# Kernel optimization log

Measured on AMD Instinct MI355X. Metric: run time of the kernel, lower is better.

## Reference

```python
import jax, jax.numpy as jnp
from jax import lax
import numpy as np

NUM_HEADS = 8
KW = 3  # window kernel size

def _avgpool3(x):
    # x: [B,C,H,W]; AvgPool2d(3,1,1) with count_include_pad=True -> sum/9
    s = lax.reduce_window(x, 0.0, lax.add, (1, 1, KW, KW), (1, 1, 1, 1),
                          ((0, 0), (0, 0), (1, 1), (1, 1)))
    return s / (KW * KW)

def _unfold3(y):
    # y: [B,h,w,C] -> [B,h,w,9,C]; patch index ordered row-major (kh,kw)
    B, h, w, C = y.shape
    yp = jnp.pad(y, ((0, 0), (1, 1), (1, 1), (0, 0)))
    return jnp.stack([yp[:, i:i + h, j:j + w, :]
                      for i in range(KW) for j in range(KW)], axis=3)

def setup_inputs():
    key = jax.random.key(0)
    ks = jax.random.split(key, 9)
    B, C, H, W = 8, 256, 64, 64
    sd = 0.02
    return {
        "x": jax.random.normal(ks[0], (B, C, H, W), jnp.float32),
        "W_qkv": jax.random.normal(ks[1], (4 * C, C), jnp.float32) * sd,
        "b_qkv": jnp.zeros((4 * C,), jnp.float32),
        "W1": jax.random.normal(ks[2], (C // 2, C), jnp.float32) * sd,
        "b1": jnp.zeros((C // 2,), jnp.float32),
        "W2": jax.random.normal(ks[3], (C, C // 2), jnp.float32) * sd,
        "b2": jnp.zeros((C,), jnp.float32),
        "Wp": jax.random.normal(ks[4], (C, C), jnp.float32) * sd,
        "bp": jnp.zeros((C,), jnp.float32),
    }

def reference(x, W_qkv, b_qkv, W1, b1, W2, b2, Wp, bp):
    B, C, H, W = x.shape
    nH = NUM_HEADS
    hd = C // nH
    scale = hd ** -0.5
    # avg pool (stride 1 keeps spatial dims), to channels-last
    y = _avgpool3(x).transpose(0, 2, 3, 1)                 # [B,h,w,C]
    qkv = y @ W_qkv.T + b_qkv                              # [B,h,w,4C]
    qkv = qkv.reshape(B, H, W, C, 4)
    q, k, v, chans = qkv[..., 0], qkv[..., 1], qkv[..., 2], qkv[..., 3]
    # channel gate
    g = jax.nn.sigmoid(jax.nn.relu(chans @ W1.T + b1) @ W2.T + b2)  # [B,h,w,C]
    # local window attention: each query attends to its 3x3 neighborhood
    qh = q.reshape(B, H, W, nH, hd)                        # [B,h,w,n,d]
    kp = _unfold3(k).reshape(B, H, W, KW * KW, nH, hd)     # [B,h,w,9,n,d]
    vp = _unfold3(v).reshape(B, H, W, KW * KW, nH, hd)
    attn = jnp.einsum('bhwnd,bhwknd->bhwnk', qh, kp) * scale
    attn = jax.nn.softmax(attn, axis=-1)
    out = jnp.einsum('bhwnk,bhwknd->bhwnd', attn, vp).reshape(B, H, W, C)
    out = out * g + out
    out = out @ Wp.T + bp
    return out.transpose(0, 3, 1, 2)                       # [B,C,H,W]
```

## Files before the change

### kernel.cpp

```cpp
#include <hip/hip_runtime.h>
#include <stdint.h>

typedef __bf16    bf16x8 __attribute__((ext_vector_type(8)));
typedef float     f32x4  __attribute__((ext_vector_type(4)));
typedef uint32_t  u32x4  __attribute__((ext_vector_type(4)));

#define MFMA(a,b,c) __builtin_amdgcn_mfma_f32_16x16x32_bf16((a),(b),(c),0,0,0)

__device__ __align__(16) uint16_t g_y [8*64*64*256];
__device__ __align__(16) uint16_t g_ao[8*64*64*256];
__device__ __align__(16) uint16_t g_ch[8*64*64*256];
__device__ __align__(16) uint16_t g_wpk[393216];

#define WQF 0
#define WKF 65536
#define WVF 131072
#define WCF 196608
#define W1F 262144
#define W2F 294912
#define WPF 327680

static __device__ __forceinline__ float b2f(uint32_t u){ return __builtin_bit_cast(float, u<<16); }
static __device__ __forceinline__ uint32_t f2b(float f){
  uint32_t x = __builtin_bit_cast(uint32_t, f);
  return (x + 0x7fffu + ((x>>16)&1u)) >> 16;
}

__global__ __launch_bounds__(256) void kpack(const float* __restrict__ Wqkv,
    const float* __restrict__ W1, const float* __restrict__ W2,
    const float* __restrict__ Wp){
  int idx = blockIdx.x*256 + threadIdx.x;
  int j = idx & 7, lane = (idx>>3)&63;
  int n16 = lane & 15, q4 = lane>>4;
  float v;
  if (idx < 262144){
    int t = idx >> 16, l = idx & 65535;
    int s = (l>>9)&7, nt = l>>12;
    v = Wqkv[(4*(nt*16+n16) + t)*256 + s*32 + q4*8 + j];
  } else if (idx < 294912){
    int l = idx - 262144;
    int s = (l>>9)&7, nt = l>>12;
    v = W1[(nt*16+n16)*256 + s*32 + q4*8 + j];
  } else if (idx < 327680){
    int l = idx - 294912;
    int s = (l>>9)&3, nt = l>>11;
    v = W2[(nt*16+n16)*128 + s*32 + q4*8 + j];
  } else {
    int l = idx - 327680;
    int s = (l>>9)&7, nt = l>>12;
    v = Wp[(nt*16+n16)*256 + s*32 + q4*8 + j];
  }
  g_wpk[idx] = (uint16_t)f2b(v);
}

__global__ __launch_bounds__(512) void kpool(const float* __restrict__ x){
  __shared__ __align__(16) uint16_t sm[3*256*82];
  uint32_t* smw = (uint32_t*)sm;
  int t = threadIdx.x;
  int b = blockIdx.x >> 6, h = blockIdx.x & 63;
  for (int i=t; i<3*256*41; i+=512) smw[i] = 0;
  __syncthreads();
  #pragma unroll
  for (int i=0;i<24;i++){
    int id = t + 512*i;
    int w4 = id&15, c = (id>>4)&255, hh = id>>12;
    int gy = h - 1 + hh;
    if ((unsigned)gy < 64u){
      f32x4 ld = *(const f32x4*)&x[(((b*256+c)*64+gy)*64) + w4*4];
      int wb = (((hh*256+c)*82 + 8 + w4*4) >> 1);
      smw[wb+0] = f2b(ld[0]) | (f2b(ld[1])<<16);
      smw[wb+1] = f2b(ld[2]) | (f2b(ld[3])<<16);
    }
  }
  __syncthreads();
  int c = t & 255, wsel = t >> 8;
  int r0 = c*82, r1 = r0 + 256*82, r2 = r1 + 256*82;
  int w0 = wsel*32;
  float csp = b2f(sm[r0+w0+7]) + b2f(sm[r1+w0+7]) + b2f(sm[r2+w0+7]);
  float csc = b2f(sm[r0+w0+8]) + b2f(sm[r1+w0+8]) + b2f(sm[r2+w0+8]);
  uint16_t* dst = g_y + ((b*64+h)*64)*256 + c;
  for (int j2=0;j2<32;j2++){
    int w = w0 + j2;
    float csn = b2f(sm[r0+w+9]) + b2f(sm[r1+w+9]) + b2f(sm[r2+w+9]);
    float yv = (csp + csc + csn) * (1.0f/9.0f);
    dst[w*256] = (uint16_t)f2b(yv);
    csp = csc; csc = csn;
  }
}

#define YSTR 264
#define HSTR 134
#define K2_QS 26400
#define K2_KS 34976
#define K2_VS 48376
__global__ __launch_bounds__(512,2) void kattn(const float* __restrict__ bqkv){
  __shared__ __align__(16) uint16_t sm[61776];
  int t = threadIdx.x;
  int lane = t & 63, wave = t >> 6;
  int n16 = lane & 15, quad = lane >> 4;
  int bb = blockIdx.x >> 6, ty = (blockIdx.x>>3)&7, tx = blockIdx.x & 7;

  {
    uint32_t* smw = (uint32_t*)sm;
    for (int i=t; i<30888; i+=512) smw[i] = 0;
  }
  __syncthreads();

  #pragma unroll
  for (int i=0;i<7;i++){
    int id = t + 512*i;
    if (id < 3200){
      int hp = id >> 5, c8 = id & 31;
      int py = hp/10, px = hp - py*10;
      int gy = ty*8 + py - 1, gx = tx*8 + px - 1;
      u32x4 ld = {0,0,0,0};
      if ((unsigned)gy<64u && (unsigned)gx<64u)
        ld = *(const u32x4*)&g_y[((bb*64+gy)*64+gx)*256 + c8*8];
      *(u32x4*)&sm[hp*YSTR + c8*8] = ld;
    }
  }
  __syncthreads();

  for (int hf=0; hf<2; hf++){
    {
      int ntg = hf*8 + wave;
      bf16x8 Bq[8];
      #pragma unroll
      for (int s=0;s<8;s++) Bq[s] = *(const bf16x8*)&g_wpk[WQF + ((ntg*8+s)*64+lane)*8];
      float bq = bqkv[4*(ntg*16+n16) + 0];
      int colB = wave*16;
      #pragma unroll
      for (int mt=0; mt<4; mt++){
        f32x4 a = {0.f,0.f,0.f,0.f};
        int m = mt*16 + n16;
        int hrow = 10*(m>>3) + (m&7) + 11;
        #pragma unroll
        for (int s=0;s<8;s++){
          bf16x8 A = *(const bf16x8*)&sm[hrow*YSTR + s*32 + quad*8];
          a = MFMA(A, Bq[s], a);
        }
        #pragma unroll
        for (int r=0;r<4;r++){
          int row = mt*16 + quad*4 + r;
          sm[K2_QS + row*HSTR + colB + n16] = (uint16_t)f2b(a[r] + bq);
        }
      }
    }
    __syncthreads();
    {
      int ntg = hf*8 + wave;
      bf16x8 Bk[8], Bv[8];
      #pragma unroll
      for (int s=0;s<8;s++){
        Bk[s] = *(const bf16x8*)&g_wpk[WKF + ((ntg*8+s)*64+lane)*8];
        Bv[s] = *(const bf16x8*)&g_wpk[WVF + ((ntg*8+s)*64+lane)*8];
      }
      float bk = bqkv[4*(ntg*16+n16) + 1];
      float bv = bqkv[4*(ntg*16+n16) + 2];
      int colB = wave*16;
      #pragma unroll
      for (int mt=0; mt<7; mt++){
        f32x4 ak = {0.f,0.f,0.f,0.f}, av = {0.f,0.f,0.f,0.f};
        int m = mt*16 + n16;
        int mr = (m < 100) ? m : 99;
        #pragma unroll
        for (int s=0;s<8;s++){
          bf16x8 A = *(const bf16x8*)&sm[mr*YSTR + s*32 + quad*8];
          ak = MFMA(A, Bk[s], ak);
          av = MFMA(A, Bv[s], av);
        }
        #pragma unroll
        for (int r=0;r<4;r++){
          int row = mt*16 + quad*4 + r;
          if (row < 100){
            int py = row/10, px = row - py*10;
            int gy = ty*8 + py - 1, gx = tx*8 + px - 1;
            bool ok = ((unsigned)gy<64u) && ((unsigned)gx<64u);
            float vk = ok ? ak[r] + bk : 0.f;
            float vv = ok ? av[r] + bv : 0.f;
            sm[K2_KS + row*HSTR + colB + n16] = (uint16_t)f2b(vk);
            sm[K2_VS + row*HSTR + colB + n16] = (uint16_t)f2b(vv);
          }
        }
      }
    }
    __syncthreads();
    if (t < 256){
      int p = t & 63, hl = t >> 6;
      int iy = p >> 3, ix = p & 7;
      int cb = hl*32;
      const uint32_t* q32 = (const uint32_t*)&sm[K2_QS + p*HSTR + cb];
      float qv[32];
      #pragma unroll
      for (int i=0;i<16;i++){ uint32_t u=q32[i]; qv[2*i]=b2f(u&0xffffu); qv[2*i+1]=b2f(u>>16); }
      int hb = (iy+1)*10 + ix + 1;
      const int off[9] = {-11,-10,-9,-1,0,1,9,10,11};
      float sc[9];
      #pragma unroll
      for (int nb=0;nb<9;nb++){
        const uint32_t* k32 = (const uint32_t*)&sm[K2_KS + (hb+off[nb])*HSTR + cb];
        float s = 0.f;
        #pragma unroll
        for (int i=0;i<16;i++){ uint32_t u=k32[i]; s += qv[2*i]*b2f(u&0xffffu) + qv[2*i+1]*b2f(u>>16); }
        sc[nb] = s * 0.17677669529663687f;
      }
      float mx = sc[0];
      #pragma unroll
      for (int nb=1;nb<9;nb++) mx = fmaxf(mx, sc[nb]);
      float l = 0.f;
      #pragma unroll
      for (int nb=0;nb<9;nb++){ sc[nb] = __expf(sc[nb]-mx); l += sc[nb]; }
      float inv = 1.f / l;
      float o[32];
      #pragma unroll
      for (int i=0;i<32;i++) o[i]=0.f;
      #pragma unroll
      for (int nb=0;nb<9;nb++){
        float wgt = sc[nb]*inv;
        const uint32_t* v32 = (const uint32_t*)&sm[K2_VS + (hb+off[nb])*HSTR + cb];
        #pragma unroll
        for (int i=0;i<16;i++){ uint32_t u=v32[i]; o[2*i] += wgt*b2f(u&0xffffu); o[2*i+1] += wgt*b2f(u>>16); }
      }
      int pg = ((bb*64 + ty*8+iy)*64 + tx*8+ix);
      uint16_t* dst = g_ao + pg*256 + hf*128 + cb;
      #pragma unroll
      for (int i=0;i<4;i++){
        u32x4 stv;
        #pragma unroll
        for (int jj=0;jj<4;jj++) stv[jj] = f2b(o[i*8+2*jj]) | (f2b(o[i*8+2*jj+1])<<16);
        *(u32x4*)&dst[i*8] = stv;
      }
    }
    __syncthreads();
  }
  #pragma unroll
  for (int jj=0;jj<2;jj++){
    int ntg = wave*2 + jj;
    bf16x8 Bc[8];
    #pragma unroll
    for (int s=0;s<8;s++) Bc[s] = *(const bf16x8*)&g_wpk[WCF + ((ntg*8+s)*64+lane)*8];
    float bc = bqkv[4*(ntg*16+n16) + 3];
    int colB = ntg*16;
    #pragma unroll
    for (int mt=0; mt<4; mt++){
      f32x4 a = {0.f,0.f,0.f,0.f};
      int m = mt*16 + n16;
      int hrow = 10*(m>>3) + (m&7) + 11;
      #pragma unroll
      for (int s=0;s<8;s++){
        bf16x8 A = *(const bf16x8*)&sm[hrow*YSTR + s*32 + quad*8];
        a = MFMA(A, Bc[s], a);
      }
      #pragma unroll
      for (int r=0;r<4;r++){
        int row = mt*16 + quad*4 + r;
        sm[K2_QS + row*264 + colB + n16] = (uint16_t)f2b(a[r] + bc);
      }
    }
  }
  __syncthreads();
  #pragma unroll
  for (int i=0;i<4;i++){
    int id = t + 512*i;
    int row = id >> 5, c8 = id & 31;
    u32x4 ld = *(const u32x4*)&sm[K2_QS + row*264 + c8*8];
    int iy = row>>3, ix = row&7;
    int pg = ((bb*64 + ty*8+iy)*64 + tx*8+ix);
    *(u32x4*)&g_ch[pg*256 + c8*8] = ld;
  }
}

#define K3_CH 0
#define K3_HS 16896
#define K3_AO 25600
__global__ __launch_bounds__(512,2) void kout(const float* __restrict__ b1,
    const float* __restrict__ b2v, const float* __restrict__ bp,
    float* __restrict__ out){
  __shared__ __align__(16) uint16_t sm[42496];
  int t = threadIdx.x;
  int lane = t & 63, wave = t >> 6;
  int n16 = lane & 15, quad = lane >> 4;
  int b = blockIdx.x >> 6, h = blockIdx.x & 63;
  int pix0 = blockIdx.x * 64;
  {
    uint32_t* smw = (uint32_t*)sm;
    for (int i=t; i<21248; i+=512) smw[i] = 0;
  }
  __syncthreads();
  #pragma unroll
  for (int i=0;i<4;i++){
    int id = t + 512*i;
    int row = id >> 5, c8 = id & 31;
    *(u32x4*)&sm[K3_CH + row*264 + c8*8] = *(const u32x4*)&g_ch[(pix0+row)*256 + c8*8];
    *(u32x4*)&sm[K3_AO + row*264 + c8*8] = *(const u32x4*)&g_ao[(pix0+row)*256 + c8*8];
  }
  __syncthreads();
  {
    int ntg = wave;
    bf16x8 Bf[8];
    #pragma unroll
    for (int s=0;s<8;s++) Bf[s] = *(const bf16x8*)&g_wpk[W1F + ((ntg*8+s)*64+lane)*8];
    float bs = b1[ntg*16+n16];
    int colB = wave*16;
    #pragma unroll
    for (int mt=0;mt<4;mt++){
      f32x4 a = {0.f,0.f,0.f,0.f};
      #pragma unroll
      for (int s=0;s<8;s++){
        bf16x8 A = *(const bf16x8*)&sm[K3_CH + (mt*16+n16)*264 + s*32 + quad*8];
        a = MFMA(A, Bf[s], a);
      }
      #pragma unroll
      for (int r=0;r<4;r++){
        int row = mt*16 + quad*4 + r;
        sm[K3_HS + row*136 + colB + n16] = (uint16_t)f2b(fmaxf(a[r]+bs, 0.f));
      }
    }
  }
  __syncthreads();
  #pragma unroll
  for (int jj=0;jj<2;jj++){
    int ntg = wave*2 + jj;
    bf16x8 Bf[4];
    #pragma unroll
    for (int s=0;s<4;s++) Bf[s] = *(const bf16x8*)&g_wpk[W2F + ((ntg*4+s)*64+lane)*8];
    float bs = b2v[ntg*16+n16];
    int colB = ntg*16;
    #pragma unroll
    for (int mt=0;mt<4;mt++){
      f32x4 a = {0.f,0.f,0.f,0.f};
      #pragma unroll
      for (int s=0;s<4;s++){
        bf16x8 A = *(const bf16x8*)&sm[K3_HS + (mt*16+n16)*136 + s*32 + quad*8];
        a = MFMA(A, Bf[s], a);
      }
      #pragma unroll
      for (int r=0;r<4;r++){
        int row = mt*16 + quad*4 + r;
        float gg = 1.f/(1.f+__expf(-(a[r] + bs)));
        float ao = b2f((uint32_t)sm[K3_AO + row*264 + colB + n16]);
        sm[K3_CH + row*264 + colB + n16] = (uint16_t)f2b(ao*(1.f+gg));
      }
    }
  }
  __syncthreads();
  #pragma unroll
  for (int jj=0;jj<2;jj++){
    int ntg = wave*2 + jj;
    bf16x8 Bf[8];
    #pragma unroll
    for (int s=0;s<8;s++) Bf[s] = *(const bf16x8*)&g_wpk[WPF + ((ntg*8+s)*64+lane)*8];
    float bs = bp[ntg*16+n16];
    int colB = ntg*16;
    #pragma unroll
    for (int mt=0;mt<4;mt++){
      f32x4 a = {0.f,0.f,0.f,0.f};
      #pragma unroll
      for (int s=0;s<8;s++){
        bf16x8 A = *(const bf16x8*)&sm[K3_CH + (mt*16+n16)*264 + s*32 + quad*8];
        a = MFMA(A, Bf[s], a);
      }
      #pragma unroll
      for (int r=0;r<4;r++){
        int row = mt*16 + quad*4 + r;
        sm[K3_AO + row*264 + colB + n16] = (uint16_t)f2b(a[r]+bs);
      }
    }
  }
  __syncthreads();
  #pragma unroll
  for (int i=0;i<8;i++){
    int idx = t + 512*i;
    int c = idx >> 4, wc = idx & 15;
    f32x4 stv;
    #pragma unroll
    for (int j=0;j<4;j++) stv[j] = b2f((uint32_t)sm[K3_AO + (wc*4+j)*264 + c]);
    *(f32x4*)&out[(((b*256)+c)*64 + h)*64 + wc*4] = stv;
  }
}

extern "C" void kernel_launch(void* const* d_in, const int* in_sizes, int n_in,
                              void* d_out, int out_size, void* d_ws, size_t ws_size,
                              hipStream_t stream){
  (void)in_sizes; (void)n_in; (void)d_ws; (void)ws_size; (void)out_size;
  const float* x    = (const float*)d_in[0];
  const float* Wqkv = (const float*)d_in[1];
  const float* bqkv = (const float*)d_in[2];
  const float* W1   = (const float*)d_in[3];
  const float* b1   = (const float*)d_in[4];
  const float* W2   = (const float*)d_in[5];
  const float* b2   = (const float*)d_in[6];
  const float* Wp   = (const float*)d_in[7];
  const float* bp   = (const float*)d_in[8];
  kpack<<<dim3(1536), dim3(256), 0, stream>>>(Wqkv, W1, W2, Wp);
  kpool<<<dim3(512),  dim3(512), 0, stream>>>(x);
  kattn<<<dim3(512),  dim3(512), 0, stream>>>(bqkv);
  kout <<<dim3(512),  dim3(512), 0, stream>>>(b1, b2, bp, (float*)d_out);
}
```

Before: 217.8 us.

## Fuse output MLP/gate/projection into attention kernel, drop global intermediates

Merges the kout kernel into kattn, so the attention output and channel-branch activations stay in registers and shared memory instead of round-tripping through the g_ao/g_ch global buffers. The channel projection now runs on waves 4-7 while waves 0-3 compute attention, overlapping the two. The change also trims the full shared-memory zeroing in kpool and kattn to only the padding that is needed, and remaps block indices for tile locality. The cost is higher register pressure from the held opk/chp arrays, and the output store is now 8x8-tile shaped, which is less contiguous.

Measured after the change: 188.4 us. 1.16x faster.

```diff
diff --git a/kernel.cpp b/kernel.cpp
--- a/kernel.cpp
+++ b/kernel.cpp
@@ -8,8 +8,6 @@
 #define MFMA(a,b,c) __builtin_amdgcn_mfma_f32_16x16x32_bf16((a),(b),(c),0,0,0)
 
 __device__ __align__(16) uint16_t g_y [8*64*64*256];
-__device__ __align__(16) uint16_t g_ao[8*64*64*256];
-__device__ __align__(16) uint16_t g_ch[8*64*64*256];
 __device__ __align__(16) uint16_t g_wpk[393216];
 
 #define WQF 0
@@ -58,8 +56,15 @@
   uint32_t* smw = (uint32_t*)sm;
   int t = threadIdx.x;
   int b = blockIdx.x >> 6, h = blockIdx.x & 63;
-  for (int i=t; i<3*256*41; i+=512) smw[i] = 0;
-  __syncthreads();
+  for (int i=t; i<768; i+=512){
+    int base = i*41;
+    smw[base+3]  = 0;
+    smw[base+36] = 0;
+  }
+  if (h==0 || h==63){
+    int hh = (h==0) ? 0 : 2;
+    for (int i=t; i<10496; i+=512) smw[hh*10496 + i] = 0;
+  }
   #pragma unroll
   for (int i=0;i<24;i++){
     int id = t + 512*i;
@@ -93,18 +98,22 @@
 #define K2_QS 26400
 #define K2_KS 34976
 #define K2_VS 48376
-__global__ __launch_bounds__(512,2) void kattn(const float* __restrict__ bqkv){
+#define MCH 0
+#define MHS 16896
+#define MAO 25600
+__global__ __launch_bounds__(512,2) void kattn(const float* __restrict__ bqkv,
+    const float* __restrict__ b1, const float* __restrict__ b2v,
+    const float* __restrict__ bp, float* __restrict__ out){
   __shared__ __align__(16) uint16_t sm[61776];
   int t = threadIdx.x;
   int lane = t & 63, wave = t >> 6;
   int n16 = lane & 15, quad = lane >> 4;
-  int bb = blockIdx.x >> 6, ty = (blockIdx.x>>3)&7, tx = blockIdx.x & 7;
-
-  {
-    uint32_t* smw = (uint32_t*)sm;
-    for (int i=t; i<30888; i+=512) smw[i] = 0;
-  }
-  __syncthreads();
+  int bid = blockIdx.x;
+  int bb = bid>>6, tyhi=(bid>>4)&3, txl=(bid>>3)&1, tylo=(bid>>2)&1, txp=bid&3;
+  int ty = tyhi*2+tylo, tx = txp*2+txl;
+
+  uint32_t opk[2][16];
+  uint32_t chp[32];
 
   #pragma unroll
   for (int i=0;i<7;i++){
@@ -121,6 +130,7 @@
   }
   __syncthreads();
 
+  #pragma unroll
   for (int hf=0; hf<2; hf++){
     {
       int ntg = hf*8 + wave;
@@ -185,8 +195,8 @@
       }
     }
     __syncthreads();
-    if (t < 256){
-      int p = t & 63, hl = t >> 6;
+    if (wave < 4){
+      int p = t & 63, hl = wave;
       int iy = p >> 3, ix = p & 7;
       int cb = hl*32;
       const uint32_t* q32 = (const uint32_t*)&sm[K2_QS + p*HSTR + cb];
@@ -221,80 +231,57 @@
         #pragma unroll
         for (int i=0;i<16;i++){ uint32_t u=v32[i]; o[2*i] += wgt*b2f(u&0xffffu); o[2*i+1] += wgt*b2f(u>>16); }
       }
-      int pg = ((bb*64 + ty*8+iy)*64 + tx*8+ix);
-      uint16_t* dst = g_ao + pg*256 + hf*128 + cb;
-      #pragma unroll
-      for (int i=0;i<4;i++){
-        u32x4 stv;
-        #pragma unroll
-        for (int jj=0;jj<4;jj++) stv[jj] = f2b(o[i*8+2*jj]) | (f2b(o[i*8+2*jj+1])<<16);
-        *(u32x4*)&dst[i*8] = stv;
+      #pragma unroll
+      for (int i=0;i<16;i++) opk[hf][i] = f2b(o[2*i]) | (f2b(o[2*i+1])<<16);
+    } else if (hf == 0){
+      #pragma unroll
+      for (int jj=0;jj<4;jj++){
+        int ntg = (wave-4)*4 + jj;
+        bf16x8 Bc[8];
+        #pragma unroll
+        for (int s=0;s<8;s++) Bc[s] = *(const bf16x8*)&g_wpk[WCF + ((ntg*8+s)*64+lane)*8];
+        float bc = bqkv[4*(ntg*16+n16) + 3];
+        #pragma unroll
+        for (int mt=0; mt<4; mt++){
+          f32x4 a = {0.f,0.f,0.f,0.f};
+          int m = mt*16 + n16;
+          int hrow = 10*(m>>3) + (m&7) + 11;
+          #pragma unroll
+          for (int s=0;s<8;s++){
+            bf16x8 A = *(const bf16x8*)&sm[hrow*YSTR + s*32 + quad*8];
+            a = MFMA(A, Bc[s], a);
+          }
+          chp[(jj*4+mt)*2+0] = f2b(a[0]+bc) | (f2b(a[1]+bc)<<16);
+          chp[(jj*4+mt)*2+1] = f2b(a[2]+bc) | (f2b(a[3]+bc)<<16);
+        }
+      }
+    } else {
+      #pragma unroll
+      for (int jj=0;jj<4;jj++){
+        int ntg = (wave-4)*4 + jj;
+        int col = ntg*16 + n16;
+        #pragma unroll
+        for (int mt=0;mt<4;mt++){
+          #pragma unroll
+          for (int r2=0;r2<2;r2++){
+            uint32_t v = chp[(jj*4+mt)*2+r2];
+            int row = mt*16 + quad*4 + r2*2;
+            sm[MCH + row*264 + col]     = (uint16_t)(v & 0xffffu);
+            sm[MCH + (row+1)*264 + col] = (uint16_t)(v >> 16);
+          }
+        }
       }
     }
     __syncthreads();
   }
-  #pragma unroll
-  for (int jj=0;jj<2;jj++){
-    int ntg = wave*2 + jj;
-    bf16x8 Bc[8];
-    #pragma unroll
-    for (int s=0;s<8;s++) Bc[s] = *(const bf16x8*)&g_wpk[WCF + ((ntg*8+s)*64+lane)*8];
-    float bc = bqkv[4*(ntg*16+n16) + 3];
-    int colB = ntg*16;
-    #pragma unroll
-    for (int mt=0; mt<4; mt++){
-      f32x4 a = {0.f,0.f,0.f,0.f};
-      int m = mt*16 + n16;
-      int hrow = 10*(m>>3) + (m&7) + 11;
-      #pragma unroll
-      for (int s=0;s<8;s++){
-        bf16x8 A = *(const bf16x8*)&sm[hrow*YSTR + s*32 + quad*8];
-        a = MFMA(A, Bc[s], a);
-      }
-      #pragma unroll
-      for (int r=0;r<4;r++){
-        int row = mt*16 + quad*4 + r;
-        sm[K2_QS + row*264 + colB + n16] = (uint16_t)f2b(a[r] + bc);
-      }
-    }
-  }
-  __syncthreads();
-  #pragma unroll
-  for (int i=0;i<4;i++){
-    int id = t + 512*i;
-    int row = id >> 5, c8 = id & 31;
-    u32x4 ld = *(const u32x4*)&sm[K2_QS + row*264 + c8*8];
-    int iy = row>>3, ix = row&7;
-    int pg = ((bb*64 + ty*8+iy)*64 + tx*8+ix);
-    *(u32x4*)&g_ch[pg*256 + c8*8] = ld;
-  }
-}
-
-#define K3_CH 0
-#define K3_HS 16896
-#define K3_AO 25600
-__global__ __launch_bounds__(512,2) void kout(const float* __restrict__ b1,
-    const float* __restrict__ b2v, const float* __restrict__ bp,
-    float* __restrict__ out){
-  __shared__ __align__(16) uint16_t sm[42496];
-  int t = threadIdx.x;
-  int lane = t & 63, wave = t >> 6;
-  int n16 = lane & 15, quad = lane >> 4;
-  int b = blockIdx.x >> 6, h = blockIdx.x & 63;
-  int pix0 = blockIdx.x * 64;
-  {
-    uint32_t* smw = (uint32_t*)sm;
-    for (int i=t; i<21248; i+=512) smw[i] = 0;
-  }
-  __syncthreads();
-  #pragma unroll
-  for (int i=0;i<4;i++){
-    int id = t + 512*i;
-    int row = id >> 5, c8 = id & 31;
-    *(u32x4*)&sm[K3_CH + row*264 + c8*8] = *(const u32x4*)&g_ch[(pix0+row)*256 + c8*8];
-    *(u32x4*)&sm[K3_AO + row*264 + c8*8] = *(const u32x4*)&g_ao[(pix0+row)*256 + c8*8];
-  }
-  __syncthreads();
+  if (wave < 4){
+    int p = t & 63, cb = wave*32;
+    #pragma unroll
+    for (int hf=0;hf<2;hf++)
+      #pragma unroll
+      for (int i=0;i<16;i++)
+        *(uint32_t*)&sm[MAO + p*264 + hf*128 + cb + 2*i] = opk[hf][i];
+  }
   {
     int ntg = wave;
     bf16x8 Bf[8];
@@ -307,13 +294,13 @@
       f32x4 a = {0.f,0.f,0.f,0.f};
       #pragma unroll
       for (int s=0;s<8;s++){
-        bf16x8 A = *(const bf16x8*)&sm[K3_CH + (mt*16+n16)*264 + s*32 + quad*8];
+        bf16x8 A = *(const bf16x8*)&sm[MCH + (mt*16+n16)*264 + s*32 + quad*8];
         a = MFMA(A, Bf[s], a);
       }
       #pragma unroll
       for (int r=0;r<4;r++){
         int row = mt*16 + quad*4 + r;
-        sm[K3_HS + row*136 + colB + n16] = (uint16_t)f2b(fmaxf(a[r]+bs, 0.f));
+        sm[MHS + row*136 + colB + n16] = (uint16_t)f2b(fmaxf(a[r]+bs, 0.f));
       }
     }
   }
@@ -331,15 +318,15 @@
       f32x4 a = {0.f,0.f,0.f,0.f};
       #pragma unroll
       for (int s=0;s<4;s++){
-        bf16x8 A = *(const bf16x8*)&sm[K3_HS + (mt*16+n16)*136 + s*32 + quad*8];
+        bf16x8 A = *(const bf16x8*)&sm[MHS + (mt*16+n16)*136 + s*32 + quad*8];
         a = MFMA(A, Bf[s], a);
       }
       #pragma unroll
       for (int r=0;r<4;r++){
         int row = mt*16 + quad*4 + r;
         float gg = 1.f/(1.f+__expf(-(a[r] + bs)));
-        float ao = b2f((uint32_t)sm[K3_AO + row*264 + colB + n16]);
-        sm[K3_CH + row*264 + colB + n16] = (uint16_t)f2b(ao*(1.f+gg));
+        float ao = b2f((uint32_t)sm[MAO + row*264 + colB + n16]);
+        sm[MCH + row*264 + colB + n16] = (uint16_t)f2b(ao*(1.f+gg));
       }
     }
   }
@@ -357,13 +344,13 @@
       f32x4 a = {0.f,0.f,0.f,0.f};
       #pragma unroll
       for (int s=0;s<8;s++){
-        bf16x8 A = *(const bf16x8*)&sm[K3_CH + (mt*16+n16)*264 + s*32 + quad*8];
+        bf16x8 A = *(const bf16x8*)&sm[MCH + (mt*16+n16)*264 + s*32 + quad*8];
         a = MFMA(A, Bf[s], a);
       }
       #pragma unroll
       for (int r=0;r<4;r++){
         int row = mt*16 + quad*4 + r;
-        sm[K3_AO + row*264 + colB + n16] = (uint16_t)f2b(a[r]+bs);
+        sm[MAO + row*264 + colB + n16] = (uint16_t)f2b(a[r]+bs);
       }
     }
   }
@@ -371,11 +358,14 @@
   #pragma unroll
   for (int i=0;i<8;i++){
     int idx = t + 512*i;
-    int c = idx >> 4, wc = idx & 15;
+    int ix4 = idx&1, iy = (idx>>1)&7, c = idx>>4;
     f32x4 stv;
     #pragma unroll
-    for (int j=0;j<4;j++) stv[j] = b2f((uint32_t)sm[K3_AO + (wc*4+j)*264 + c]);
-    *(f32x4*)&out[(((b*256)+c)*64 + h)*64 + wc*4] = stv;
+    for (int j=0;j<4;j++){
+      int p = iy*8 + ix4*4 + j;
+      stv[j] = b2f((uint32_t)sm[MAO + p*264 + c]);
+    }
+    *(f32x4*)&out[(((bb*256+c)*64) + ty*8+iy)*64 + tx*8 + ix4*4] = stv;
   }
 }
 
@@ -394,6 +384,5 @@
   const float* bp   = (const float*)d_in[8];
   kpack<<<dim3(1536), dim3(256), 0, stream>>>(Wqkv, W1, W2, Wp);
   kpool<<<dim3(512),  dim3(512), 0, stream>>>(x);
-  kattn<<<dim3(512),  dim3(512), 0, stream>>>(bqkv);
-  kout <<<dim3(512),  dim3(512), 0, stream>>>(b1, b2, bp, (float*)d_out);
-}
+  kattn<<<dim3(512),  dim3(512), 0, stream>>>(bqkv, b1, b2, bp, (float*)d_out);
+}
```
